# Performance work log

Hardware: AMD Instinct MI355X
Metric: run time of the kernel (lower is better)

## Reference

```python
import jax, jax.numpy as jnp
import numpy as np

N, C, HID, FEAT = 4096, 1024, 512, 128
KS = (5, 10, 15)  # k values used when k == -1 (hyedge_concat path)


def _sq_cdist(x):
    # squared pairwise euclidean distances; monotone in torch.cdist for topk
    n = (x * x).sum(-1)
    d2 = n[:, None] + n[None, :] - 2.0 * (x @ x.T)
    return jnp.maximum(d2, 0.0)


def neighbor_distance(x, k):
    # k nearest neighbors (smallest distance, self included) -> incidence H [N, N]
    # hyperedge e (column) = neighborhood of node e
    _, idx = jax.lax.top_k(-_sq_cdist(x), k)  # [N, k]
    n = x.shape[0]
    H = jnp.zeros((n, n), x.dtype).at[idx, jnp.arange(n)[:, None]].set(1.0)
    return H


def build_H(x, k):
    if k == -1:  # k is a static Python int
        return jnp.concatenate([neighbor_distance(x, kk) for kk in KS], axis=1)
    return neighbor_distance(x, k)


def hyconv(x, H, W):
    Dv = H.sum(1)  # node degree [N]
    De = H.sum(0)  # edge degree [E]
    dv = jnp.where(Dv > 0, 1.0 / jnp.sqrt(Dv), 0.0)
    de = jnp.where(De > 0, 1.0 / De, 0.0)
    m = (H.T @ (x * dv[:, None])) * de[:, None]  # [E, C]
    return ((H @ m) * dv[:, None]) @ W


def feat_model(x, H, W1, W2):
    return hyconv(jax.nn.relu(hyconv(x, H, W1)), H, W2)


def setup_inputs() -> dict:
    key = jax.random.key(0)
    k1, k2, k3, k4 = jax.random.split(key, 4)
    return {
        "fts_gt": jax.random.normal(k1, (N, C), jnp.float32),
        "fts1": jax.random.normal(k2, (N, C), jnp.float32),
        "W1": jax.random.normal(k3, (C, HID), jnp.float32) / np.sqrt(C).astype(np.float32),
        "W2": jax.random.normal(k4, (HID, FEAT), jnp.float32) / np.sqrt(HID).astype(np.float32),
        "k": -1,
    }


def reference(fts_gt, fts1, W1, W2, k):
    H_gt = build_H(fts_gt, k)
    H1 = build_H(fts1, k)
    feat_gt = feat_model(fts_gt, H_gt, W1, W2)  # [N, FEAT]
    feat1 = feat_model(fts1, H1, W1, W2)
    # sensitive == 'attribute': mean over node dim
    feat_gt = feat_gt.mean(axis=0)
    feat1 = feat1.mean(axis=0)
    y0 = feat_gt.sum()
    y1 = feat1.sum()
    y_compare = (feat_gt[None] - feat1[None]).sum()[None]  # shape [1]
    return (jax.nn.sigmoid(y_compare), y0, y1)
```

## Files before the change

kernel.cpp:

```cpp
#include <hip/hip_runtime.h>
#include <math.h>


#define NN   4096
#define CC   1024
#define HIDN 512
#define FEATN 128
#define NE   12288
#define KTOT 30
#define KMAX 15
#define CH   16
#define MAXCH (NN + NN * KTOT / CH)

typedef __attribute__((ext_vector_type(4))) int i32x4;
typedef unsigned short ushort_t;

__device__ __forceinline__ unsigned short bf16_rne(float x) {
    unsigned u = __float_as_uint(x);
    unsigned r = (u + 0x7FFFu + ((u >> 16) & 1u)) >> 16;
    return (unsigned short)r;
}
__device__ __forceinline__ float bf16_lo(unsigned u) { return __uint_as_float(u << 16); }
__device__ __forceinline__ float bf16_hi(unsigned u) { return __uint_as_float(u & 0xFFFF0000u); }
__device__ __forceinline__ unsigned packbf(float a, float b) {
    return (unsigned)bf16_rne(a) | ((unsigned)bf16_rne(b) << 16);
}

__device__ __forceinline__ void async16(void* lds, const void* g) {
    __builtin_amdgcn_global_load_lds((const __attribute__((address_space(1))) unsigned int*)g,
                                     (__attribute__((address_space(3))) unsigned int*)lds, 16, 0, 0);
}

__global__ __launch_bounds__(256) void k_rownorm2(const float* __restrict__ X,
                                                  float* __restrict__ nrm,
                                                  float* __restrict__ qs) {
    __shared__ float s[256];
    __shared__ float sm[256];
    int i = blockIdx.x, t = threadIdx.x;
    const float* row = X + (size_t)i * CC;
    float acc = 0.f, mx = 0.f;
#pragma unroll
    for (int j = 0; j < CC / 256; ++j) {
        float v = row[t + 256 * j];
        acc += v * v;
        mx = fmaxf(mx, fabsf(v));
    }
    s[t] = acc; sm[t] = mx; __syncthreads();
    for (int d = 128; d > 0; d >>= 1) {
        if (t < d) { s[t] += s[t + d]; sm[t] = fmaxf(sm[t], sm[t + d]); }
        __syncthreads();
    }
    if (t == 0) { nrm[i] = s[0]; qs[i] = fmaxf(sm[0], 1e-20f) / 127.0f; }
}

__global__ __launch_bounds__(256) void k_quant(const float* __restrict__ X,
                                               const float* __restrict__ qs,
                                               signed char* __restrict__ H,
                                               signed char* __restrict__ L) {
    int p = blockIdx.x * 256 + threadIdx.x;
    int i = p >> 8;
    float inv = 1.0f / qs[i];
    float4 v = *reinterpret_cast<const float4*>(&X[(size_t)p * 4]);
    float f[4] = { v.x, v.y, v.z, v.w };
    char hh[4], ll[4];
#pragma unroll
    for (int j = 0; j < 4; ++j) {
        float xs = f[j] * inv;
        float h = rintf(xs);
        float l = rintf((xs - h) * 128.0f);
        hh[j] = (char)(int)h;
        ll[j] = (char)(int)l;
    }
    *reinterpret_cast<char4*>(&H[(size_t)p * 4]) = make_char4(hh[0], hh[1], hh[2], hh[3]);
    *reinterpret_cast<char4*>(&L[(size_t)p * 4]) = make_char4(ll[0], ll[1], ll[2], ll[3]);
}

__global__ __launch_bounds__(256) void k_w1max(const float* __restrict__ W,
                                               float* __restrict__ sig) {
    __shared__ float s[256];
    int t = threadIdx.x;
    int col = blockIdx.x * 64 + (t & 63);
    int seg = t >> 6;
    float mx = 0.f;
    for (int k = seg * 256; k < seg * 256 + 256; ++k)
        mx = fmaxf(mx, fabsf(W[(size_t)k * HIDN + col]));
    s[t] = mx; __syncthreads();
    if (seg == 0) {
        mx = fmaxf(fmaxf(s[t], s[t + 64]), fmaxf(s[t + 128], s[t + 192]));
        sig[col] = fmaxf(mx, 1e-20f) / 127.0f;
    }
}

__global__ __launch_bounds__(256) void k_wt8(const float* __restrict__ W,
                                             const float* __restrict__ sig,
                                             signed char* __restrict__ Th,
                                             signed char* __restrict__ Tl) {
    __shared__ float s[32][33];
    int bx = blockIdx.x, by = blockIdx.y;
    int tx = threadIdx.x & 31, ty = threadIdx.x >> 5;
#pragma unroll
    for (int rr = 0; rr < 4; ++rr) {
        int k = by * 32 + ty + rr * 8;
        s[ty + rr * 8][tx] = W[(size_t)k * HIDN + bx * 32 + tx];
    }
    __syncthreads();
#pragma unroll
    for (int rr = 0; rr < 4; ++rr) {
        int n = bx * 32 + ty + rr * 8;
        int k = by * 32 + tx;
        float x = s[tx][ty + rr * 8];
        float xs = x / sig[n];
        float h = rintf(xs);
        float l = rintf((xs - h) * 128.0f);
        Th[(size_t)n * CC + k] = (char)(int)h;
        Tl[(size_t)n * CC + k] = (char)(int)l;
    }
}

__global__ __launch_bounds__(256) void k_w2bar(const float* __restrict__ W2,
                                               float* __restrict__ wbar) {
    int k = blockIdx.x * 256 + threadIdx.x;
    const float* row = W2 + (size_t)k * FEATN;
    float s = 0.f;
#pragma unroll
    for (int f = 0; f < FEATN; f += 4) {
        float4 v = *reinterpret_cast<const float4*>(&row[f]);
        s += v.x + v.y + v.z + v.w;
    }
    wbar[k] = s;
}

template <bool SYM, bool OUTB>
__global__ __launch_bounds__(256) void k_mm8(const signed char* __restrict__ Ah,
                                             const signed char* __restrict__ Al,
                                             const signed char* __restrict__ Bh,
                                             const signed char* __restrict__ Bl,
                                             const float* __restrict__ rs,
                                             const float* __restrict__ cs,
                                             float* __restrict__ C,
                                             ushort_t* __restrict__ Cb, int ldc) {
    int bi, bj;
    if (SYM) {
        int b0 = (int)blockIdx.x;
        int L = (b0 & 7) * 66 + (b0 >> 3);
        int rem = L, si = 0;
        for (; si < 8; ++si) {
            int grp = 10 + (7 - si) * 16;
            if (rem < grp) break;
            rem -= grp;
        }
        int sj, u, v;
        if (rem < 10) {
            int uu = 0, r2 = rem;
            while (r2 >= 4 - uu) { r2 -= 4 - uu; ++uu; }
            u = uu; v = uu + r2; sj = si;
        } else {
            int r2 = rem - 10;
            sj = si + 1 + (r2 >> 4);
            int w2 = r2 & 15;
            u = w2 >> 2; v = w2 & 3;
        }
        bi = si * 4 + u; bj = sj * 4 + v;
    } else {
        bi = blockIdx.y; bj = blockIdx.x;
    }
    __shared__ char smem[SYM ? 128 * 129 * 4 : 4 * 128 * 64];
    char (*lds)[128][64] = reinterpret_cast<char(*)[128][64]>(smem);
    int t = threadIdx.x;
    int w = t >> 6, l = t & 63;
    int wr = (w >> 1) * 64, wc = (w & 1) * 64;

    i32x4 acc1[4][4], acc2[4][4];
#pragma unroll
    for (int i = 0; i < 4; ++i)
#pragma unroll
        for (int j = 0; j < 4; ++j) { acc1[i][j] = (i32x4){0,0,0,0}; acc2[i][j] = (i32x4){0,0,0,0}; }

    const signed char* src[4] = {
        Ah + (size_t)bi * 128 * 1024,
        Al + (size_t)bi * 128 * 1024,
        Bh + (size_t)bj * 128 * 1024,
        Bl + (size_t)bj * 128 * 1024
    };
    int srow = l >> 2;
    int sslot = (l & 3) ^ ((l >> 3) & 3);

    int col = l & 15;
    int kg = l >> 4;

    for (int kt = 0; kt < 16; ++kt) {
        int k0 = kt * 64;
#pragma unroll
        for (int q = 0; q < 4; ++q) {
#pragma unroll
            for (int s2 = 0; s2 < 2; ++s2) {
                int rbase = (w * 2 + s2) * 16;
                const signed char* g = src[q] + (size_t)(rbase + srow) * 1024 + k0 + sslot * 16;
                async16(&lds[q][rbase][0], g);
            }
        }
        __syncthreads();
        i32x4 ah[4], al4[4], bh4[4], bl4[4];
#pragma unroll
        for (int mi = 0; mi < 4; ++mi) {
            int row = wr + mi * 16 + col;
            int ph = kg ^ ((row >> 1) & 3);
            ah[mi]  = *reinterpret_cast<const i32x4*>(&lds[0][row][ph * 16]);
            al4[mi] = *reinterpret_cast<const i32x4*>(&lds[1][row][ph * 16]);
        }
#pragma unroll
        for (int nj = 0; nj < 4; ++nj) {
            int row = wc + nj * 16 + col;
            int ph = kg ^ ((row >> 1) & 3);
            bh4[nj] = *reinterpret_cast<const i32x4*>(&lds[2][row][ph * 16]);
            bl4[nj] = *reinterpret_cast<const i32x4*>(&lds[3][row][ph * 16]);
        }
#pragma unroll
        for (int mi = 0; mi < 4; ++mi)
#pragma unroll
            for (int nj = 0; nj < 4; ++nj) {
                acc1[mi][nj] = __builtin_amdgcn_mfma_i32_16x16x64_i8(ah[mi], bh4[nj], acc1[mi][nj], 0, 0, 0);
                acc2[mi][nj] = __builtin_amdgcn_mfma_i32_16x16x64_i8(ah[mi], bl4[nj], acc2[mi][nj], 0, 0, 0);
                acc2[mi][nj] = __builtin_amdgcn_mfma_i32_16x16x64_i8(al4[mi], bh4[nj], acc2[mi][nj], 0, 0, 0);
            }
        __syncthreads();
    }

    float* fl = reinterpret_cast<float*>(smem);
#pragma unroll
    for (int mi = 0; mi < 4; ++mi) {
#pragma unroll
        for (int r = 0; r < 4; ++r) {
            int rl = wr + mi * 16 + (l >> 4) * 4 + r;
            int rg = bi * 128 + rl;
            float rsv = rs[rg];
#pragma unroll
            for (int nj = 0; nj < 4; ++nj) {
                int cl = wc + nj * 16 + col;
                int cg = bj * 128 + cl;
                float v = ((float)acc1[mi][nj][r] + (float)acc2[mi][nj][r] * (1.0f / 128.0f))
                          * rsv * cs[cg];
                if (OUTB) {
                    Cb[(size_t)rg * ldc + cg] = bf16_rne(v);
                } else {
                    C[(size_t)rg * ldc + cg] = v;
                    if (SYM && bi != bj) fl[cl * 129 + rl] = v;
                }
            }
        }
    }
    if (SYM && !OUTB && bi != bj) {
        __syncthreads();
#pragma unroll 4
        for (int it = 0; it < 64; ++it) {
            int row = it * 2 + (t >> 7);
            int c2 = t & 127;
            C[(size_t)(bj * 128 + row) * ldc + bi * 128 + c2] = fl[row * 129 + c2];
        }
    }
}

__global__ __launch_bounds__(256) void k_topk(const float* __restrict__ G,
                                              const float* __restrict__ nrm,
                                              int* __restrict__ idx_out) {
    __shared__ unsigned long long wsm[4];
    int e = blockIdx.x, t = threadIdx.x;
    float ne = nrm[e];
    const float* Grow = G + (size_t)e * NN;
    unsigned long long key[16];
    unsigned long long my = ~0ull;
#pragma unroll
    for (int j = 0; j < 16; ++j) {
        int i = t + 256 * j;
        float v = fmaxf(ne + nrm[i] - 2.0f * Grow[i], 0.0f);
        unsigned long long k = ((unsigned long long)__float_as_uint(v) << 32) | (unsigned)i;
        key[j] = k;
        my = k < my ? k : my;
    }
    for (int r = 0; r < KMAX; ++r) {
        unsigned long long m = my;
#pragma unroll
        for (int d = 1; d < 64; d <<= 1) {
            unsigned long long o = __shfl_xor(m, d);
            m = o < m ? o : m;
        }
        if ((t & 63) == 0) wsm[t >> 6] = m;
        __syncthreads();
        unsigned long long b0 = wsm[0] < wsm[1] ? wsm[0] : wsm[1];
        unsigned long long b1 = wsm[2] < wsm[3] ? wsm[2] : wsm[3];
        unsigned long long bk = b0 < b1 ? b0 : b1;
        int win = (int)(unsigned)bk;
        if (t == 0) idx_out[e * 16 + r] = win;
        if (t == (win & 255)) {
            int jw = win >> 8;
#pragma unroll
            for (int jj = 0; jj < 16; ++jj) if (jj == jw) key[jj] = ~0ull;
            my = ~0ull;
#pragma unroll
            for (int jj = 0; jj < 16; ++jj) my = key[jj] < my ? key[jj] : my;
        }
        __syncthreads();
    }
}

__device__ __forceinline__ void decode_pair(int p, int& e, int& b, int& j) {
    e = p / KTOT;
    int q = p - e * KTOT;
    if (q < 5)       { b = 0; j = q; }
    else if (q < 15) { b = 1; j = q - 5; }
    else             { b = 2; j = q - 15; }
}

__global__ __launch_bounds__(256) void k_count(const int* __restrict__ idx, int* __restrict__ Dv) {
    int p = blockIdx.x * 256 + threadIdx.x;
    int e, b, j; decode_pair(p, e, b, j);
    (void)b;
    atomicAdd(&Dv[idx[e * 16 + j]], 1);
}

__global__ __launch_bounds__(256) void k_dv(const int* __restrict__ Dv,
                                            const float* __restrict__ qs,
                                            float* __restrict__ dvv,
                                            float* __restrict__ rs1) {
    int i = blockIdx.x * 256 + threadIdx.x;
    int d = Dv[i];
    float dv = d > 0 ? 1.0f / sqrtf((float)d) : 0.0f;
    dvv[i] = dv;
    rs1[i] = dv * qs[i];
}

__global__ __launch_bounds__(1024) void k_scan(const int* __restrict__ Dv,
                                               int* __restrict__ offs,
                                               int* __restrict__ cur,
                                               int* __restrict__ chunkoffs,
                                               int* __restrict__ nchunks) {
    __shared__ int s[1024];
    int t = threadIdx.x;
    int v[4]; int sum = 0;
#pragma unroll
    for (int j = 0; j < 4; ++j) { v[j] = Dv[t * 4 + j]; sum += v[j]; }
    s[t] = sum; __syncthreads();
    for (int d = 1; d < 1024; d <<= 1) {
        int add = (t >= d) ? s[t - d] : 0;
        __syncthreads();
        s[t] += add;
        __syncthreads();
    }
    int run = s[t] - sum;
#pragma unroll
    for (int j = 0; j < 4; ++j) { offs[t * 4 + j] = run; cur[t * 4 + j] = run; run += v[j]; }
    if (t == 1023) offs[NN] = run;
    __syncthreads();
    int c[4]; int csum = 0;
#pragma unroll
    for (int j = 0; j < 4; ++j) { c[j] = (v[j] + CH - 1) / CH; csum += c[j]; }
    s[t] = csum; __syncthreads();
    for (int d = 1; d < 1024; d <<= 1) {
        int add = (t >= d) ? s[t - d] : 0;
        __syncthreads();
        s[t] += add;
        __syncthreads();
    }
    int crun = s[t] - csum;
#pragma unroll
    for (int j = 0; j < 4; ++j) { chunkoffs[t * 4 + j] = crun; crun += c[j]; }
    if (t == 1023) { chunkoffs[NN] = crun; *nchunks = crun; }
}

__global__ __launch_bounds__(256) void k_fill(const int* __restrict__ idx,
                                              int* __restrict__ cur,
                                              int* __restrict__ adj) {
    int p = blockIdx.x * 256 + threadIdx.x;
    int e, b, j; decode_pair(p, e, b, j);
    int i = idx[e * 16 + j];
    int eg = b * NN + e;
    int pos = atomicAdd(&cur[i], 1);
    adj[pos] = eg;
}

__global__ __launch_bounds__(256) void k_tasks(const int* __restrict__ chunkoffs,
                                               int* __restrict__ task_node) {
    int i = blockIdx.x * 256 + threadIdx.x;
    int c0 = chunkoffs[i], c1 = chunkoffs[i + 1];
    for (int c = c0; c < c1; ++c) task_node[c] = i;
}

__global__ __launch_bounds__(256) void k_ze(const int* __restrict__ idx,
                                            const float* __restrict__ dvv,
                                            float* __restrict__ ze) {
    int eg = blockIdx.x * 256 + threadIdx.x;
    int b = eg >> 12, e = eg & (NN - 1);
    int kb = (b == 0) ? 5 : (b == 1) ? 10 : 15;
    const int* row = idx + e * 16;
    float s = 0.f;
    for (int j = 0; j < kb; ++j) s += dvv[row[j]];
    ze[eg] = s / (float)kb;
}

__global__ __launch_bounds__(256) void k_ascat(const int* __restrict__ idx,
                                               const float* __restrict__ ze,
                                               float* __restrict__ a) {
    int p = blockIdx.x * 256 + threadIdx.x;
    int e, b, j; decode_pair(p, e, b, j);
    atomicAdd(&a[idx[e * 16 + j]], ze[b * NN + e]);
}

__global__ __launch_bounds__(256) void k_edge3(const int* __restrict__ idx,
                                               const ushort_t* __restrict__ t1b,
                                               ushort_t* __restrict__ m) {
    int p = blockIdx.x * 256 + threadIdx.x;
    int e = p >> 6;
    int c8 = (p & 63) * 8;
    const int* row = idx + e * 16;
    float acc[8] = {};
    auto addrow = [&](int j) {
        uint4 raw = *reinterpret_cast<const uint4*>(&t1b[(size_t)row[j] * HIDN + c8]);
        acc[0] += bf16_lo(raw.x); acc[1] += bf16_hi(raw.x);
        acc[2] += bf16_lo(raw.y); acc[3] += bf16_hi(raw.y);
        acc[4] += bf16_lo(raw.z); acc[5] += bf16_hi(raw.z);
        acc[6] += bf16_lo(raw.w); acc[7] += bf16_hi(raw.w);
    };
    auto store = [&](size_t eg, float sc) {
        uint4 o;
        o.x = packbf(acc[0] * sc, acc[1] * sc);
        o.y = packbf(acc[2] * sc, acc[3] * sc);
        o.z = packbf(acc[4] * sc, acc[5] * sc);
        o.w = packbf(acc[6] * sc, acc[7] * sc);
        *reinterpret_cast<uint4*>(&m[eg * HIDN + c8]) = o;
    };
#pragma unroll
    for (int j = 0; j < 5; ++j) addrow(j);
    store((size_t)e, 0.2f);
#pragma unroll
    for (int j = 5; j < 10; ++j) addrow(j);
    store((size_t)(NN + e), 0.1f);
#pragma unroll
    for (int j = 10; j < 15; ++j) addrow(j);
    store((size_t)(2 * NN + e), 1.0f / 15.0f);
}

__global__ __launch_bounds__(256) void k_chunk(const int* __restrict__ offs,
                                               const int* __restrict__ chunkoffs,
                                               const int* __restrict__ task_node,
                                               const int* __restrict__ nchunks,
                                               const int* __restrict__ adj,
                                               const ushort_t* __restrict__ m,
                                               float* __restrict__ partial) {
    int task = blockIdx.x * 4 + threadIdx.x / 64;
    if (task >= *nchunks) return;
    int c8 = (threadIdx.x & 63) * 8;
    int i = task_node[task];
    int ck = task - chunkoffs[i];
    int q0 = offs[i] + ck * CH;
    int n = offs[i + 1] - q0;
    n = n < CH ? n : CH;
    int e[CH];
#pragma unroll
    for (int j = 0; j < CH; ++j) e[j] = (j < n) ? adj[q0 + j] : -1;
    float acc[8] = {};
#pragma unroll
    for (int j = 0; j < CH; ++j) {
        if (e[j] >= 0) {
            uint4 raw = *reinterpret_cast<const uint4*>(&m[(size_t)e[j] * HIDN + c8]);
            acc[0] += bf16_lo(raw.x); acc[1] += bf16_hi(raw.x);
            acc[2] += bf16_lo(raw.y); acc[3] += bf16_hi(raw.y);
            acc[4] += bf16_lo(raw.z); acc[5] += bf16_hi(raw.z);
            acc[6] += bf16_lo(raw.w); acc[7] += bf16_hi(raw.w);
        }
    }
    float* o = &partial[(size_t)task * HIDN + c8];
    *reinterpret_cast<float4*>(o)     = make_float4(acc[0], acc[1], acc[2], acc[3]);
    *reinterpret_cast<float4*>(o + 4) = make_float4(acc[4], acc[5], acc[6], acc[7]);
}

__global__ __launch_bounds__(256) void k_comb2(const int* __restrict__ chunkoffs,
                                               const float* __restrict__ dvv,
                                               const float* __restrict__ a,
                                               const float* __restrict__ wbar,
                                               const float* __restrict__ partial,
                                               float* __restrict__ g) {
    __shared__ float s[256];
    int p = blockIdx.x * 256 + threadIdx.x;
    int i = p >> 7;
    int c4 = (p & 127) * 4;
    int c0 = chunkoffs[i], c1 = chunkoffs[i + 1];
    float4 acc = make_float4(0.f, 0.f, 0.f, 0.f);
    for (int c = c0; c < c1; ++c) {
        float4 v = *reinterpret_cast<const float4*>(&partial[(size_t)c * HIDN + c4]);
        acc.x += v.x; acc.y += v.y; acc.z += v.z; acc.w += v.w;
    }
    float dv = dvv[i];
    float4 wv = *reinterpret_cast<const float4*>(&wbar[c4]);
    float val = fmaxf(acc.x * dv, 0.f) * wv.x + fmaxf(acc.y * dv, 0.f) * wv.y +
                fmaxf(acc.z * dv, 0.f) * wv.z + fmaxf(acc.w * dv, 0.f) * wv.w;
    int t = threadIdx.x;
    s[t] = val; __syncthreads();
    for (int d = 64; d > 0; d >>= 1) {
        if ((t & 127) < d) s[t] += s[t + d];
        __syncthreads();
    }
    if ((t & 127) == 0) g[i] = s[t] * dv * a[i];
}

__global__ __launch_bounds__(1024) void k_yred(const float* __restrict__ g,
                                               float* __restrict__ ys, int slot) {
    __shared__ float s[1024];
    int t = threadIdx.x;
    s[t] = g[t] + g[t + 1024] + g[t + 2048] + g[t + 3072];
    __syncthreads();
    for (int d = 512; d > 0; d >>= 1) { if (t < d) s[t] += s[t + d]; __syncthreads(); }
    if (t == 0) ys[slot] = s[0];
}

__global__ void k_fin(const float* __restrict__ ys, float* __restrict__ out) {
    float y0 = ys[0] / (float)NN, y1 = ys[1] / (float)NN;
    out[0] = 1.0f / (1.0f + expf(-(y0 - y1)));
    out[1] = y0;
    out[2] = y1;
}

extern "C" void kernel_launch(void* const* d_in, const int* in_sizes, int n_in,
                              void* d_out, int out_size, void* d_ws, size_t ws_size,
                              hipStream_t stream) {
    const float* fts[2] = { (const float*)d_in[0], (const float*)d_in[1] };
    const float* W1 = (const float*)d_in[2];
    const float* W2 = (const float*)d_in[3];
    float* out = (float*)d_out;

    char* p = (char*)d_ws;
    auto alloc = [&](size_t b) { char* r = p; p += (b + 255) & ~(size_t)255; return r; };
    float* G    = (float*)alloc((size_t)NN * NN * 4);
    float* nrm  = (float*)alloc((size_t)NN * 4);
    float* qs   = (float*)alloc((size_t)NN * 4);
    int*   idx  = (int*)  alloc((size_t)NN * 16 * 4);
    int*   Dv   = (int*)  alloc((size_t)NN * 4);
    float* dvv  = (float*)alloc((size_t)NN * 4);
    float* rs1  = (float*)alloc((size_t)NN * 4);
    int*   offs = (int*)  alloc((size_t)(NN + 1) * 4);
    int*   cur  = (int*)  alloc((size_t)NN * 4);
    int*   coffs= (int*)  alloc((size_t)(NN + 1) * 4);
    int*   nch  = (int*)  alloc(4);
    int*   tnode= (int*)  alloc((size_t)MAXCH * 4);
    int*   adj  = (int*)  alloc((size_t)NN * KTOT * 4);
    signed char* Xqh = (signed char*)alloc((size_t)NN * CC);
    signed char* Xql = (signed char*)alloc((size_t)NN * CC);
    signed char* Wqh = (signed char*)alloc((size_t)HIDN * CC);
    signed char* Wql = (signed char*)alloc((size_t)HIDN * CC);
    float* w1sig = (float*)alloc((size_t)HIDN * 4);
    ushort_t* t1b = (ushort_t*)alloc((size_t)NN * HIDN * 2);
    ushort_t* m   = (ushort_t*)alloc((size_t)NE * HIDN * 2);
    float* wbar = (float*)alloc((size_t)HIDN * 4);
    float* ze   = (float*)alloc((size_t)NE * 4);
    float* a    = (float*)alloc((size_t)NN * 4);
    float* g    = (float*)alloc((size_t)NN * 4);
    float* ys   = (float*)alloc(2 * 4);

    float* partial = G;

    k_w1max<<<HIDN / 64, 256, 0, stream>>>(W1, w1sig);
    k_wt8<<<dim3(HIDN / 32, CC / 32), 256, 0, stream>>>(W1, w1sig, Wqh, Wql);
    k_w2bar<<<HIDN / 256, 256, 0, stream>>>(W2, wbar);

    for (int s = 0; s < 2; ++s) {
        const float* X = fts[s];
        k_rownorm2<<<NN, 256, 0, stream>>>(X, nrm, qs);
        k_quant<<<NN * CC / 4 / 256, 256, 0, stream>>>(X, qs, Xqh, Xql);
        k_mm8<true, false><<<528, 256, 0, stream>>>(Xqh, Xql, Xqh, Xql, qs, qs, G, nullptr, NN);
        k_topk<<<NN, 256, 0, stream>>>(G, nrm, idx);
        hipMemsetAsync(Dv, 0, NN * 4, stream);
        k_count<<<NN * KTOT / 256, 256, 0, stream>>>(idx, Dv);
        k_dv<<<NN / 256, 256, 0, stream>>>(Dv, qs, dvv, rs1);
        k_scan<<<1, 1024, 0, stream>>>(Dv, offs, cur, coffs, nch);
        k_fill<<<NN * KTOT / 256, 256, 0, stream>>>(idx, cur, adj);
        k_tasks<<<NN / 256, 256, 0, stream>>>(coffs, tnode);
        k_ze<<<NE / 256, 256, 0, stream>>>(idx, dvv, ze);
        hipMemsetAsync(a, 0, NN * 4, stream);
        k_ascat<<<NN * KTOT / 256, 256, 0, stream>>>(idx, ze, a);
        k_mm8<false, true><<<dim3(HIDN / 128, NN / 128), 256, 0, stream>>>(Xqh, Xql, Wqh, Wql, rs1, w1sig, nullptr, t1b, HIDN);
        k_edge3<<<NN * 64 / 256, 256, 0, stream>>>(idx, t1b, m);
        k_chunk<<<(MAXCH + 3) / 4, 256, 0, stream>>>(offs, coffs, tnode, nch, adj, m, partial);
        k_comb2<<<NN * 128 / 256, 256, 0, stream>>>(coffs, dvv, a, wbar, partial, g);
        k_yred<<<1, 1024, 0, stream>>>(g, ys, s);
    }
    k_fin<<<1, 1, 0, stream>>>(ys, out);
}
```

Before: 737.6 us.

## Double-buffer int8 MFMA GEMM LDS tiles and write symmetric transpose directly

The int8 split-precision GEMM now keeps two LDS buffers. It issues the async loads for the next K tile before computing the current one, which removes the load-then-sync stall on every iteration. The epilogue no longer stages the transposed tile through LDS for the symmetric mirror write. Each lane writes its four values as a float4 straight into the transposed location. This doubles LDS use to 64KB per block, which may cut occupancy, and the direct transposed stores are less coalesced.

After: 625.4 us. 1.18x faster.

```diff
diff --git a/kernel.cpp b/kernel.cpp
--- a/kernel.cpp
+++ b/kernel.cpp
@@ -164,8 +164,7 @@
     } else {
         bi = blockIdx.y; bj = blockIdx.x;
     }
-    __shared__ char smem[SYM ? 128 * 129 * 4 : 4 * 128 * 64];
-    char (*lds)[128][64] = reinterpret_cast<char(*)[128][64]>(smem);
+    __shared__ char smem[2][4][128][64];
     int t = threadIdx.x;
     int w = t >> 6, l = t & 63;
     int wr = (w >> 1) * 64, wc = (w & 1) * 64;
@@ -188,7 +187,7 @@
     int col = l & 15;
     int kg = l >> 4;
 
-    for (int kt = 0; kt < 16; ++kt) {
+    auto stage = [&](int buf, int kt) {
         int k0 = kt * 64;
 #pragma unroll
         for (int q = 0; q < 4; ++q) {
@@ -196,24 +195,30 @@
             for (int s2 = 0; s2 < 2; ++s2) {
                 int rbase = (w * 2 + s2) * 16;
                 const signed char* g = src[q] + (size_t)(rbase + srow) * 1024 + k0 + sslot * 16;
-                async16(&lds[q][rbase][0], g);
+                async16(&smem[buf][q][rbase][0], g);
             }
         }
-        __syncthreads();
+    };
+
+    stage(0, 0);
+    __syncthreads();
+    int cur = 0;
+    for (int kt = 0; kt < 16; ++kt) {
+        if (kt + 1 < 16) stage(cur ^ 1, kt + 1);
         i32x4 ah[4], al4[4], bh4[4], bl4[4];
 #pragma unroll
         for (int mi = 0; mi < 4; ++mi) {
             int row = wr + mi * 16 + col;
             int ph = kg ^ ((row >> 1) & 3);
-            ah[mi]  = *reinterpret_cast<const i32x4*>(&lds[0][row][ph * 16]);
-            al4[mi] = *reinterpret_cast<const i32x4*>(&lds[1][row][ph * 16]);
+            ah[mi]  = *reinterpret_cast<const i32x4*>(&smem[cur][0][row][ph * 16]);
+            al4[mi] = *reinterpret_cast<const i32x4*>(&smem[cur][1][row][ph * 16]);
         }
 #pragma unroll
         for (int nj = 0; nj < 4; ++nj) {
             int row = wc + nj * 16 + col;
             int ph = kg ^ ((row >> 1) & 3);
-            bh4[nj] = *reinterpret_cast<const i32x4*>(&lds[2][row][ph * 16]);
-            bl4[nj] = *reinterpret_cast<const i32x4*>(&lds[3][row][ph * 16]);
+            bh4[nj] = *reinterpret_cast<const i32x4*>(&smem[cur][2][row][ph * 16]);
+            bl4[nj] = *reinterpret_cast<const i32x4*>(&smem[cur][3][row][ph * 16]);
         }
 #pragma unroll
         for (int mi = 0; mi < 4; ++mi)
@@ -224,38 +229,33 @@
                 acc2[mi][nj] = __builtin_amdgcn_mfma_i32_16x16x64_i8(al4[mi], bh4[nj], acc2[mi][nj], 0, 0, 0);
             }
         __syncthreads();
-    }
-
-    float* fl = reinterpret_cast<float*>(smem);
+        cur ^= 1;
+    }
+
 #pragma unroll
     for (int mi = 0; mi < 4; ++mi) {
-#pragma unroll
-        for (int r = 0; r < 4; ++r) {
-            int rl = wr + mi * 16 + (l >> 4) * 4 + r;
-            int rg = bi * 128 + rl;
-            float rsv = rs[rg];
-#pragma unroll
-            for (int nj = 0; nj < 4; ++nj) {
-                int cl = wc + nj * 16 + col;
-                int cg = bj * 128 + cl;
-                float v = ((float)acc1[mi][nj][r] + (float)acc2[mi][nj][r] * (1.0f / 128.0f))
-                          * rsv * cs[cg];
-                if (OUTB) {
-                    Cb[(size_t)rg * ldc + cg] = bf16_rne(v);
-                } else {
-                    C[(size_t)rg * ldc + cg] = v;
-                    if (SYM && bi != bj) fl[cl * 129 + rl] = v;
-                }
+        int rg0 = bi * 128 + wr + mi * 16 + (l >> 4) * 4;
+#pragma unroll
+        for (int nj = 0; nj < 4; ++nj) {
+            int cg = bj * 128 + wc + nj * 16 + col;
+            float csv = cs[cg];
+            float vr[4];
+#pragma unroll
+            for (int r = 0; r < 4; ++r)
+                vr[r] = ((float)acc1[mi][nj][r] + (float)acc2[mi][nj][r] * (1.0f / 128.0f))
+                        * rs[rg0 + r] * csv;
+            if (OUTB) {
+#pragma unroll
+                for (int r = 0; r < 4; ++r)
+                    Cb[(size_t)(rg0 + r) * ldc + cg] = bf16_rne(vr[r]);
+            } else {
+#pragma unroll
+                for (int r = 0; r < 4; ++r)
+                    C[(size_t)(rg0 + r) * ldc + cg] = vr[r];
+                if (SYM && bi != bj)
+                    *reinterpret_cast<float4*>(&C[(size_t)cg * ldc + rg0]) =
+                        make_float4(vr[0], vr[1], vr[2], vr[3]);
             }
-        }
-    }
-    if (SYM && !OUTB && bi != bj) {
-        __syncthreads();
-#pragma unroll 4
-        for (int it = 0; it < 64; ++it) {
-            int row = it * 2 + (t >> 7);
-            int c2 = t & 127;
-            C[(size_t)(bj * 128 + row) * ldc + bi * 128 + c2] = fl[row * 129 + c2];
         }
     }
 }
```
